# Performance work log

Measured on AMD Instinct MI355X. Metric: run time of the kernel, lower is better.

The kernel has to match this reference:

```python
import jax, jax.numpy as jnp
import numpy as np

DIM_OUT = 64


def setup_inputs() -> dict:
    key = jax.random.key(0)
    k1, k2, k3, k4 = jax.random.split(key, 4)
    B, N, D_in, D_out = 4, 4096, 512, DIM_OUT
    x = jax.random.normal(k1, (B, N, D_in), dtype=jnp.float32)
    s = 1.0 / np.sqrt(D_in)
    Wk = jax.random.normal(k2, (D_out, D_in), dtype=jnp.float32) * s
    Wq = jax.random.normal(k3, (D_out, D_in), dtype=jnp.float32) * s
    Wv = jax.random.normal(k4, (D_out, D_in), dtype=jnp.float32) * s
    return {"x": x, "Wk": Wk, "Wq": Wq, "Wv": Wv}


def reference(x, Wk, Wq, Wv):
    # x: [B, N, D_in]; W*: [D_out, D_in] (torch Linear, no bias -> x @ W.T)
    keys = jnp.einsum('bnd,od->bno', x, Wk)
    queries = jnp.einsum('bnd,od->bno', x, Wq)
    values = jnp.einsum('bnd,od->bno', x, Wv)
    d_out = Wk.shape[0]
    # causal attention scores: [B, N, N]
    scores = jnp.einsum('bio,bjo->bij', queries, keys) / jnp.sqrt(jnp.float32(d_out))
    N = x.shape[1]
    causal = jnp.tril(jnp.ones((N, N), dtype=bool))  # [N, N]
    scores = jnp.where(causal[None, :, :], scores, -jnp.inf)
    att = jax.nn.softmax(scores, axis=-1)
    return jnp.einsum('bjo,bij->bio', values, att)
```

## Files before the change

kernel.cpp:

```cpp
#include <hip/hip_runtime.h>
#include <hip/hip_bf16.h>
#include <math.h>

#define N_   4096
#define DIN  512
#define D_   64

typedef __attribute__((ext_vector_type(8))) short  bf16x8;
typedef __attribute__((ext_vector_type(4))) float  f32x4;

__device__ __forceinline__ unsigned short bf16rne(float x) {
    unsigned u = __float_as_uint(x);
    return (unsigned short)((u + 0x7FFFu + ((u >> 16) & 1u)) >> 16);
}
__device__ __forceinline__ unsigned cvt2(float a, float b) {
    __hip_bfloat162 h = __float22bfloat162_rn(make_float2(a, b));
    unsigned u; __builtin_memcpy(&u, &h, 4);
    return u;
}
__device__ __forceinline__ uint2 cvt4(float4 v) {
    return make_uint2(cvt2(v.x, v.y), cvt2(v.z, v.w));
}
__device__ __forceinline__ int swz(int row, int byte_in_row) {
    return (row * 128 + (byte_in_row ^ ((row & 7) << 4))) >> 1;
}

__device__ __forceinline__ int pb64(int qi) {
    const int k = qi >> 4;
    return qi + 16 * (k * (k - 1) / 2) + (qi & 15) * k;
}

#define PART64_F 4160

__global__ __launch_bounds__(512) void proj_kernel(
    const float* __restrict__ X, const float* __restrict__ Wk,
    const float* __restrict__ Wq, const float* __restrict__ Wv,
    unsigned short* __restrict__ Kb, unsigned short* __restrict__ Qb,
    unsigned short* __restrict__ Vt)
{
    __shared__ unsigned short Xs[2][64 * 64];
    __shared__ unsigned short Ws[2][192 * 64];

    const int tid  = threadIdx.x;
    const int lane = tid & 63;
    const int w    = tid >> 6;
    const int q15  = lane & 15;
    const int hi   = lane >> 4;
    const int rt   = w >> 1;
    const int oh   = w & 1;
    const int rbase = blockIdx.x * 64;

    float4 xr[2], wr[6];

    auto loadT = [&](int kc) {
        #pragma unroll
        for (int i = 0; i < 2; ++i) {
            const int idx = tid + i * 512;
            xr[i] = *(const float4*)(X + (size_t)(rbase + (idx >> 4)) * DIN + kc + (idx & 15) * 4);
        }
        #pragma unroll
        for (int i = 0; i < 6; ++i) {
            const int idx  = tid + i * 512;
            const int wrow = idx >> 4;
            const float* Wp = (wrow < 64)  ? Wk + (size_t)wrow * DIN
                            : (wrow < 128) ? Wq + (size_t)(wrow - 64) * DIN
                                           : Wv + (size_t)(wrow - 128) * DIN;
            wr[i] = *(const float4*)(Wp + kc + (idx & 15) * 4);
        }
    };
    auto storeT = [&](int p) {
        #pragma unroll
        for (int i = 0; i < 2; ++i) {
            const int idx = tid + i * 512;
            *(uint2*)&Xs[p][swz(idx >> 4, (idx & 15) * 8)] = cvt4(xr[i]);
        }
        #pragma unroll
        for (int i = 0; i < 6; ++i) {
            const int idx = tid + i * 512;
            *(uint2*)&Ws[p][swz(idx >> 4, (idx & 15) * 8)] = cvt4(wr[i]);
        }
    };

    f32x4 acc[6];
    #pragma unroll
    for (int i = 0; i < 6; ++i) acc[i] = (f32x4){0.f, 0.f, 0.f, 0.f};

    loadT(0);
    int p = 0;
    for (int it = 0; it < 8; ++it) {
        storeT(p);
        __syncthreads();
        if (it < 7) loadT((it + 1) * 64);
        #pragma unroll
        for (int ks = 0; ks < 2; ++ks) {
            bf16x8 af = *(const bf16x8*)&Xs[p][swz(rt * 16 + q15, ks * 64 + hi * 16)];
            #pragma unroll
            for (int j = 0; j < 6; ++j) {
                bf16x8 bfr = *(const bf16x8*)&Ws[p][swz((oh * 6 + j) * 16 + q15, ks * 64 + hi * 16)];
                acc[j] = __builtin_amdgcn_mfma_f32_16x16x32_bf16(af, bfr, acc[j], 0, 0, 0);
            }
        }
        p ^= 1;
    }

    unsigned short* Os = &Ws[0][0];
    #pragma unroll
    for (int j = 0; j < 6; ++j) {
        const int og = oh * 6 + j;
        #pragma unroll
        for (int r = 0; r < 4; ++r) {
            const int n = rt * 16 + hi * 4 + r;
            const int o = og * 16 + q15;
            unsigned short v = bf16rne(acc[j][r]);
            if (og < 4)      Kb[(size_t)(rbase + n) * D_ + o]        = v;
            else if (og < 8) Qb[(size_t)(rbase + n) * D_ + (o - 64)] = v;
            else             Os[n * 66 + (o - 128)]                  = v;
        }
    }
    __syncthreads();
    {
        const int o  = tid >> 3;
        const int ng = (tid & 7) * 8;
        unsigned short tmp[8];
        #pragma unroll
        for (int i = 0; i < 8; ++i) tmp[i] = Os[(ng + i) * 66 + o];
        const int b  = rbase >> 12;
        const int nb = rbase & (N_ - 1);
        *(uint4*)(Vt + ((size_t)b * D_ + o) * N_ + nb + ng) = *(uint4*)&tmp[0];
    }
}

__global__ __launch_bounds__(256, 3) void attn_part_kernel(
    const unsigned short* __restrict__ Qb, const unsigned short* __restrict__ Kb,
    const unsigned short* __restrict__ Vt, float* __restrict__ Pws)
{
    __shared__ unsigned short Ks[2][64 * 64];
    __shared__ unsigned short Vs[2][64 * 64];
    __shared__ unsigned short Pb[4][16 * 64];

    const int tid  = threadIdx.x;
    const int lane = tid & 63;
    const int w    = tid >> 6;
    const int q15  = lane & 15;
    const int hi   = lane >> 4;

    const int b = blockIdx.x & 3;
    const int u = blockIdx.x >> 2;
    int sl, qi;
    if      (u < 64)  { sl = 0; qi = 63 - u; }
    else if (u < 112) { sl = 1; qi = 63 - (u - 64); }
    else if (u < 144) { sl = 2; qi = 63 - (u - 112); }
    else              { sl = 3; qi = 63 - (u - 144); }
    const int nch  = qi + 1;
    const int cbeg = sl * 16;
    const int cend = min(nch, cbeg + 16);

    const unsigned short* Qp = Qb + (size_t)b * N_ * D_;
    const unsigned short* Kp = Kb + (size_t)b * N_ * D_;
    const unsigned short* Vp = Vt + (size_t)b * D_ * N_;

    const int qg = qi * 64 + w * 16 + q15;
    bf16x8 qf[2];
    #pragma unroll
    for (int ks = 0; ks < 2; ++ks)
        qf[ks] = *(const bf16x8*)(Qp + (size_t)qg * D_ + ks * 32 + hi * 8);

    f32x4 accO[4];
    #pragma unroll
    for (int dt = 0; dt < 4; ++dt) accO[dt] = (f32x4){0.f, 0.f, 0.f, 0.f};
    float lsum = 0.f;

    const int srow = tid >> 2;
    const int sb0  = (tid & 3) * 32;
    uint4 kr0, kr1, vr0, vr1;

    auto loadC = [&](int c) {
        const int kb2 = c * 64;
        const unsigned short* kp = Kp + (size_t)(kb2 + srow) * D_ + sb0 / 2;
        kr0 = *(const uint4*)kp;
        kr1 = *(const uint4*)(kp + 8);
        const unsigned short* vp = Vp + (size_t)srow * N_ + kb2 + sb0 / 2;
        vr0 = *(const uint4*)vp;
        vr1 = *(const uint4*)(vp + 8);
    };
    auto writeC = [&](int p) {
        *(uint4*)&Ks[p][swz(srow, sb0)]      = kr0;
        *(uint4*)&Ks[p][swz(srow, sb0 + 16)] = kr1;
        *(uint4*)&Vs[p][swz(srow, sb0)]      = vr0;
        *(uint4*)&Vs[p][swz(srow, sb0 + 16)] = vr1;
    };

    loadC(cbeg);
    writeC(0);
    __syncthreads();

    unsigned short* Pw = &Pb[w][0];
    const float SC = 0.125f * 1.44269504f;
    int p = 0;

    for (int c = cbeg; c < cend; ++c) {
        const int kbase = c * 64;
        if (c + 1 < cend) loadC(c + 1);

        f32x4 sv[4];
        #pragma unroll
        for (int kt = 0; kt < 4; ++kt) {
            bf16x8 k0 = *(const bf16x8*)&Ks[p][swz(kt * 16 + q15, hi * 16)];
            bf16x8 k1 = *(const bf16x8*)&Ks[p][swz(kt * 16 + q15, 64 + hi * 16)];
            sv[kt] = __builtin_amdgcn_mfma_f32_16x16x32_bf16(k0, qf[0], (f32x4){0.f,0.f,0.f,0.f}, 0, 0, 0);
            sv[kt] = __builtin_amdgcn_mfma_f32_16x16x32_bf16(k1, qf[1], sv[kt], 0, 0, 0);
        }

        #pragma unroll
        for (int kt = 0; kt < 4; ++kt) {
            float pv[4];
            #pragma unroll
            for (int r = 0; r < 4; ++r) {
                float v = sv[kt][r] * SC;
                const int kg = kbase + kt * 16 + hi * 4 + r;
                v = (kg <= qg) ? v : -INFINITY;
                pv[r] = __builtin_amdgcn_exp2f(v);
                lsum += pv[r];
            }
            *(uint2*)&Pw[swz(q15, kt * 32 + hi * 8)] =
                make_uint2(cvt2(pv[0], pv[1]), cvt2(pv[2], pv[3]));
        }

        #pragma unroll
        for (int ks2 = 0; ks2 < 2; ++ks2) {
            bf16x8 pf = *(const bf16x8*)&Pw[swz(q15, ks2 * 64 + hi * 16)];
            #pragma unroll
            for (int dt = 0; dt < 4; ++dt) {
                bf16x8 vf = *(const bf16x8*)&Vs[p][swz(dt * 16 + q15, ks2 * 64 + hi * 16)];
                accO[dt] = __builtin_amdgcn_mfma_f32_16x16x32_bf16(vf, pf, accO[dt], 0, 0, 0);
            }
        }

        __syncthreads();
        if (c + 1 < cend) writeC(p ^ 1);
        __syncthreads();
        p ^= 1;
    }

    lsum += __shfl_xor(lsum, 16);
    lsum += __shfl_xor(lsum, 32);

    float* partO = Pws + ((size_t)b * 160 + pb64(qi) + sl) * PART64_F;
    #pragma unroll
    for (int dt = 0; dt < 4; ++dt)
        #pragma unroll
        for (int r = 0; r < 4; ++r)
            partO[(dt * 16 + hi * 4 + r) * 64 + w * 16 + q15] = accO[dt][r];
    if (hi == 0) partO[4096 + w * 16 + q15] = lsum;
}

__global__ __launch_bounds__(256) void attn_merge_kernel(
    const float* __restrict__ Pws, float* __restrict__ O)
{
    __shared__ float Tr[64 * 68];
    __shared__ float Ls[64];

    const int tid = threadIdx.x;
    const int b   = blockIdx.x & 3;
    const int qi  = blockIdx.x >> 2;
    const int np  = (qi + 16) >> 4;
    const float* base = Pws + ((size_t)b * 160 + pb64(qi)) * PART64_F;

    {
        const int d  = tid >> 2;
        const int qg = (tid & 3) * 16;
        float s[16];
        #pragma unroll
        for (int i = 0; i < 16; ++i) s[i] = 0.f;
        for (int pp = 0; pp < np; ++pp) {
            const float* sp = base + (size_t)pp * PART64_F + d * 64 + qg;
            #pragma unroll
            for (int i = 0; i < 4; ++i) {
                float4 v = *(const float4*)(sp + i * 4);
                s[4*i]   += v.x; s[4*i+1] += v.y;
                s[4*i+2] += v.z; s[4*i+3] += v.w;
            }
        }
        #pragma unroll
        for (int i = 0; i < 16; ++i) Tr[d * 68 + qg + i] = s[i];
    }
    if (tid < 64) {
        float L = 0.f;
        for (int pp = 0; pp < np; ++pp) L += base[(size_t)pp * PART64_F + 4096 + tid];
        Ls[tid] = 1.0f / L;
    }
    __syncthreads();
    {
        const int q  = tid >> 2;
        const int dg = (tid & 3) * 16;
        const float rL = Ls[q];
        float ov[16];
        #pragma unroll
        for (int i = 0; i < 16; ++i) ov[i] = Tr[(dg + i) * 68 + q] * rL;
        float* dst = O + ((size_t)b * N_ + qi * 64 + q) * D_ + dg;
        #pragma unroll
        for (int i = 0; i < 4; ++i)
            *(float4*)(dst + i * 4) = make_float4(ov[4*i], ov[4*i+1], ov[4*i+2], ov[4*i+3]);
    }
}

extern "C" void kernel_launch(void* const* d_in, const int* in_sizes, int n_in,
                              void* d_out, int out_size, void* d_ws, size_t ws_size,
                              hipStream_t stream)
{
    const float* x  = (const float*)d_in[0];
    const float* Wk = (const float*)d_in[1];
    const float* Wq = (const float*)d_in[2];
    const float* Wv = (const float*)d_in[3];
    float* O = (float*)d_out;

    const size_t per = (size_t)4 * N_ * D_;
    unsigned short* Kb = (unsigned short*)d_ws;
    unsigned short* Qb = Kb + per;
    unsigned short* Vt = Qb + per;
    float* Pws = (float*)((char*)d_ws + 3 * per * sizeof(unsigned short));

    proj_kernel<<<dim3(4 * N_ / 64), 512, 0, stream>>>(x, Wk, Wq, Wv, Kb, Qb, Vt);
    attn_part_kernel<<<dim3(640), 256, 0, stream>>>(Qb, Kb, Vt, Pws);
    attn_merge_kernel<<<dim3(256), 256, 0, stream>>>(Pws, O);
}
```

Baseline: 51.56 us.

## Use 128-query attention tiles with direct global-to-LDS K/V loads

Each attention block now covers 128 query rows instead of 64, with each wave handling two 16-row query tiles. Every K/V chunk staged in shared memory therefore feeds twice as many MFMAs, halving K/V traffic per query. K/V chunks are loaded with global_load_lds straight into pre-swizzled LDS, replacing register staging and dropping one barrier per iteration. The causal mask is applied only on the diagonal chunks. The partial-sum layout and the merge kernel are reworked for 128-row tiles. The trade-off is half as many blocks (320 partial, 128 merge), which may leave CUs idle or unbalanced, plus higher register and LDS use per block.

```diff
diff --git a/kernel.cpp b/kernel.cpp
--- a/kernel.cpp
+++ b/kernel.cpp
@@ -8,6 +8,8 @@
 
 typedef __attribute__((ext_vector_type(8))) short  bf16x8;
 typedef __attribute__((ext_vector_type(4))) float  f32x4;
+
+#define ZERO4 ((f32x4){0.f, 0.f, 0.f, 0.f})
 
 __device__ __forceinline__ unsigned short bf16rne(float x) {
     unsigned u = __float_as_uint(x);
@@ -25,12 +27,16 @@
     return (row * 128 + (byte_in_row ^ ((row & 7) << 4))) >> 1;
 }
 
-__device__ __forceinline__ int pb64(int qi) {
-    const int k = qi >> 4;
-    return qi + 16 * (k * (k - 1) / 2) + (qi & 15) * k;
-}
-
-#define PART64_F 4160
+#define GLD16(gp, lp)                                                          \
+    __builtin_amdgcn_global_load_lds(                                          \
+        (const __attribute__((address_space(1))) unsigned int*)(gp),           \
+        (__attribute__((address_space(3))) unsigned int*)(lp), 16, 0, 0)
+
+__device__ __forceinline__ int pb128(int qi) {
+    const int g = qi >> 3, r = qi & 7;
+    return 4 * g * (g + 1) + r * (g + 1);
+}
+#define PART128_F 8320
 
 __global__ __launch_bounds__(512) void proj_kernel(
     const float* __restrict__ X, const float* __restrict__ Wk,
@@ -83,7 +89,7 @@
 
     f32x4 acc[6];
     #pragma unroll
-    for (int i = 0; i < 6; ++i) acc[i] = (f32x4){0.f, 0.f, 0.f, 0.f};
+    for (int i = 0; i < 6; ++i) acc[i] = ZERO4;
 
     loadT(0);
     int p = 0;
@@ -130,13 +136,13 @@
     }
 }
 
-__global__ __launch_bounds__(256, 3) void attn_part_kernel(
+__global__ __launch_bounds__(256) void attn_part_kernel(
     const unsigned short* __restrict__ Qb, const unsigned short* __restrict__ Kb,
     const unsigned short* __restrict__ Vt, float* __restrict__ Pws)
 {
     __shared__ unsigned short Ks[2][64 * 64];
     __shared__ unsigned short Vs[2][64 * 64];
-    __shared__ unsigned short Pb[4][16 * 64];
+    __shared__ unsigned short Pb[4][32 * 64];
 
     const int tid  = threadIdx.x;
     const int lane = tid & 63;
@@ -147,51 +153,47 @@
     const int b = blockIdx.x & 3;
     const int u = blockIdx.x >> 2;
     int sl, qi;
-    if      (u < 64)  { sl = 0; qi = 63 - u; }
-    else if (u < 112) { sl = 1; qi = 63 - (u - 64); }
-    else if (u < 144) { sl = 2; qi = 63 - (u - 112); }
-    else              { sl = 3; qi = 63 - (u - 144); }
-    const int nch  = qi + 1;
+    if      (u < 32) { sl = 0; qi = 31 - u; }
+    else if (u < 56) { sl = 1; qi = 31 - (u - 32); }
+    else if (u < 72) { sl = 2; qi = 31 - (u - 56); }
+    else             { sl = 3; qi = 31 - (u - 72); }
+    const int nch  = 2 * qi + 2;
     const int cbeg = sl * 16;
     const int cend = min(nch, cbeg + 16);
+    const int qb   = qi * 128;
 
     const unsigned short* Qp = Qb + (size_t)b * N_ * D_;
     const unsigned short* Kp = Kb + (size_t)b * N_ * D_;
     const unsigned short* Vp = Vt + (size_t)b * D_ * N_;
 
-    const int qg = qi * 64 + w * 16 + q15;
-    bf16x8 qf[2];
-    #pragma unroll
-    for (int ks = 0; ks < 2; ++ks)
-        qf[ks] = *(const bf16x8*)(Qp + (size_t)qg * D_ + ks * 32 + hi * 8);
-
-    f32x4 accO[4];
-    #pragma unroll
-    for (int dt = 0; dt < 4; ++dt) accO[dt] = (f32x4){0.f, 0.f, 0.f, 0.f};
-    float lsum = 0.f;
-
-    const int srow = tid >> 2;
-    const int sb0  = (tid & 3) * 32;
-    uint4 kr0, kr1, vr0, vr1;
-
-    auto loadC = [&](int c) {
+    bf16x8 qf[2][2];
+    #pragma unroll
+    for (int qq = 0; qq < 2; ++qq)
+        #pragma unroll
+        for (int ks = 0; ks < 2; ++ks)
+            qf[qq][ks] = *(const bf16x8*)(Qp + (size_t)(qb + w * 32 + qq * 16 + q15) * D_ + ks * 32 + hi * 8);
+
+    f32x4 accO[2][4];
+    #pragma unroll
+    for (int qq = 0; qq < 2; ++qq)
+        #pragma unroll
+        for (int dt = 0; dt < 4; ++dt) accO[qq][dt] = ZERO4;
+    float lsum[2] = {0.f, 0.f};
+
+    const int lsw = 8 * ((lane & 7) ^ (lane >> 3));
+
+    auto issueChunk = [&](int p, int c) {
         const int kb2 = c * 64;
-        const unsigned short* kp = Kp + (size_t)(kb2 + srow) * D_ + sb0 / 2;
-        kr0 = *(const uint4*)kp;
-        kr1 = *(const uint4*)(kp + 8);
-        const unsigned short* vp = Vp + (size_t)srow * N_ + kb2 + sb0 / 2;
-        vr0 = *(const uint4*)vp;
-        vr1 = *(const uint4*)(vp + 8);
+        #pragma unroll
+        for (int i = 0; i < 2; ++i) {
+            const int r8  = w * 2 + i;
+            const int row = r8 * 8 + (lane >> 3);
+            GLD16(Kp + (size_t)(kb2 + row) * D_ + lsw, &Ks[p][r8 * 512]);
+            GLD16(Vp + (size_t)row * N_ + kb2 + lsw,   &Vs[p][r8 * 512]);
+        }
     };
-    auto writeC = [&](int p) {
-        *(uint4*)&Ks[p][swz(srow, sb0)]      = kr0;
-        *(uint4*)&Ks[p][swz(srow, sb0 + 16)] = kr1;
-        *(uint4*)&Vs[p][swz(srow, sb0)]      = vr0;
-        *(uint4*)&Vs[p][swz(srow, sb0 + 16)] = vr1;
-    };
-
-    loadC(cbeg);
-    writeC(0);
+
+    issueChunk(0, cbeg);
     __syncthreads();
 
     unsigned short* Pw = &Pb[w][0];
@@ -199,108 +201,126 @@
     int p = 0;
 
     for (int c = cbeg; c < cend; ++c) {
+        if (c + 1 < cend) issueChunk(p ^ 1, c + 1);
         const int kbase = c * 64;
-        if (c + 1 < cend) loadC(c + 1);
-
-        f32x4 sv[4];
+        const bool edge = (c >= nch - 2);
+
+        f32x4 sv[2][4];
         #pragma unroll
         for (int kt = 0; kt < 4; ++kt) {
             bf16x8 k0 = *(const bf16x8*)&Ks[p][swz(kt * 16 + q15, hi * 16)];
             bf16x8 k1 = *(const bf16x8*)&Ks[p][swz(kt * 16 + q15, 64 + hi * 16)];
-            sv[kt] = __builtin_amdgcn_mfma_f32_16x16x32_bf16(k0, qf[0], (f32x4){0.f,0.f,0.f,0.f}, 0, 0, 0);
-            sv[kt] = __builtin_amdgcn_mfma_f32_16x16x32_bf16(k1, qf[1], sv[kt], 0, 0, 0);
-        }
-
-        #pragma unroll
-        for (int kt = 0; kt < 4; ++kt) {
-            float pv[4];
-            #pragma unroll
-            for (int r = 0; r < 4; ++r) {
-                float v = sv[kt][r] * SC;
-                const int kg = kbase + kt * 16 + hi * 4 + r;
-                v = (kg <= qg) ? v : -INFINITY;
-                pv[r] = __builtin_amdgcn_exp2f(v);
-                lsum += pv[r];
+            sv[0][kt] = __builtin_amdgcn_mfma_f32_16x16x32_bf16(k0, qf[0][0], ZERO4, 0, 0, 0);
+            sv[0][kt] = __builtin_amdgcn_mfma_f32_16x16x32_bf16(k1, qf[0][1], sv[0][kt], 0, 0, 0);
+            sv[1][kt] = __builtin_amdgcn_mfma_f32_16x16x32_bf16(k0, qf[1][0], ZERO4, 0, 0, 0);
+            sv[1][kt] = __builtin_amdgcn_mfma_f32_16x16x32_bf16(k1, qf[1][1], sv[1][kt], 0, 0, 0);
+        }
+
+        #pragma unroll
+        for (int qq = 0; qq < 2; ++qq) {
+            const int qg = qb + w * 32 + qq * 16 + q15;
+            #pragma unroll
+            for (int kt = 0; kt < 4; ++kt) {
+                float pv[4];
+                #pragma unroll
+                for (int r = 0; r < 4; ++r) {
+                    float v = sv[qq][kt][r] * SC;
+                    const int kg = kbase + kt * 16 + hi * 4 + r;
+                    if (edge) v = (kg <= qg) ? v : -INFINITY;
+                    pv[r] = __builtin_amdgcn_exp2f(v);
+                    lsum[qq] += pv[r];
+                }
+                *(uint2*)&Pw[swz(qq * 16 + q15, kt * 32 + hi * 8)] =
+                    make_uint2(cvt2(pv[0], pv[1]), cvt2(pv[2], pv[3]));
             }
-            *(uint2*)&Pw[swz(q15, kt * 32 + hi * 8)] =
-                make_uint2(cvt2(pv[0], pv[1]), cvt2(pv[2], pv[3]));
         }
 
         #pragma unroll
         for (int ks2 = 0; ks2 < 2; ++ks2) {
-            bf16x8 pf = *(const bf16x8*)&Pw[swz(q15, ks2 * 64 + hi * 16)];
-            #pragma unroll
-            for (int dt = 0; dt < 4; ++dt) {
-                bf16x8 vf = *(const bf16x8*)&Vs[p][swz(dt * 16 + q15, ks2 * 64 + hi * 16)];
-                accO[dt] = __builtin_amdgcn_mfma_f32_16x16x32_bf16(vf, pf, accO[dt], 0, 0, 0);
+            bf16x8 vf[4];
+            #pragma unroll
+            for (int dt = 0; dt < 4; ++dt)
+                vf[dt] = *(const bf16x8*)&Vs[p][swz(dt * 16 + q15, ks2 * 64 + hi * 16)];
+            #pragma unroll
+            for (int qq = 0; qq < 2; ++qq) {
+                bf16x8 pf = *(const bf16x8*)&Pw[swz(qq * 16 + q15, ks2 * 64 + hi * 16)];
+                #pragma unroll
+                for (int dt = 0; dt < 4; ++dt)
+                    accO[qq][dt] = __builtin_amdgcn_mfma_f32_16x16x32_bf16(vf[dt], pf, accO[qq][dt], 0, 0, 0);
             }
         }
 
-        __syncthreads();
-        if (c + 1 < cend) writeC(p ^ 1);
         __syncthreads();
         p ^= 1;
     }
 
-    lsum += __shfl_xor(lsum, 16);
-    lsum += __shfl_xor(lsum, 32);
-
-    float* partO = Pws + ((size_t)b * 160 + pb64(qi) + sl) * PART64_F;
-    #pragma unroll
-    for (int dt = 0; dt < 4; ++dt)
-        #pragma unroll
-        for (int r = 0; r < 4; ++r)
-            partO[(dt * 16 + hi * 4 + r) * 64 + w * 16 + q15] = accO[dt][r];
-    if (hi == 0) partO[4096 + w * 16 + q15] = lsum;
+    #pragma unroll
+    for (int qq = 0; qq < 2; ++qq) {
+        lsum[qq] += __shfl_xor(lsum[qq], 16);
+        lsum[qq] += __shfl_xor(lsum[qq], 32);
+    }
+
+    float* partO = Pws + ((size_t)b * 80 + pb128(qi) + sl) * PART128_F;
+    #pragma unroll
+    for (int qq = 0; qq < 2; ++qq) {
+        #pragma unroll
+        for (int dt = 0; dt < 4; ++dt)
+            #pragma unroll
+            for (int r = 0; r < 4; ++r)
+                partO[(dt * 16 + hi * 4 + r) * 128 + w * 32 + qq * 16 + q15] = accO[qq][dt][r];
+        if (hi == 0) partO[8192 + w * 32 + qq * 16 + q15] = lsum[qq];
+    }
 }
 
 __global__ __launch_bounds__(256) void attn_merge_kernel(
     const float* __restrict__ Pws, float* __restrict__ O)
 {
-    __shared__ float Tr[64 * 68];
-    __shared__ float Ls[64];
+    __shared__ float Tr[64 * 132];
+    __shared__ float Ls[128];
 
     const int tid = threadIdx.x;
     const int b   = blockIdx.x & 3;
     const int qi  = blockIdx.x >> 2;
-    const int np  = (qi + 16) >> 4;
-    const float* base = Pws + ((size_t)b * 160 + pb64(qi)) * PART64_F;
+    const int np  = (qi >> 3) + 1;
+    const float* base = Pws + ((size_t)b * 80 + pb128(qi)) * PART128_F;
 
     {
         const int d  = tid >> 2;
-        const int qg = (tid & 3) * 16;
-        float s[16];
-        #pragma unroll
-        for (int i = 0; i < 16; ++i) s[i] = 0.f;
+        const int qg = (tid & 3) * 32;
+        float s[32];
+        #pragma unroll
+        for (int i = 0; i < 32; ++i) s[i] = 0.f;
         for (int pp = 0; pp < np; ++pp) {
-            const float* sp = base + (size_t)pp * PART64_F + d * 64 + qg;
-            #pragma unroll
-            for (int i = 0; i < 4; ++i) {
+            const float* sp = base + (size_t)pp * PART128_F + d * 128 + qg;
+            #pragma unroll
+            for (int i = 0; i < 8; ++i) {
                 float4 v = *(const float4*)(sp + i * 4);
                 s[4*i]   += v.x; s[4*i+1] += v.y;
                 s[4*i+2] += v.z; s[4*i+3] += v.w;
             }
         }
         #pragma unroll
-        for (int i = 0; i < 16; ++i) Tr[d * 68 + qg + i] = s[i];
-    }
-    if (tid < 64) {
+        for (int i = 0; i < 32; ++i) Tr[d * 132 + qg + i] = s[i];
+    }
+    if (tid < 128) {
         float L = 0.f;
-        for (int pp = 0; pp < np; ++pp) L += base[(size_t)pp * PART64_F + 4096 + tid];
+        for (int pp = 0; pp < np; ++pp) L += base[(size_t)pp * PART128_F + 8192 + tid];
         Ls[tid] = 1.0f / L;
     }
     __syncthreads();
     {
-        const int q  = tid >> 2;
-        const int dg = (tid & 3) * 16;
+        const int q  = tid >> 1;
+        const int dg = (tid & 1) * 32;
         const float rL = Ls[q];
-        float ov[16];
-        #pragma unroll
-        for (int i = 0; i < 16; ++i) ov[i] = Tr[(dg + i) * 68 + q] * rL;
-        float* dst = O + ((size_t)b * N_ + qi * 64 + q) * D_ + dg;
-        #pragma unroll
-        for (int i = 0; i < 4; ++i)
-            *(float4*)(dst + i * 4) = make_float4(ov[4*i], ov[4*i+1], ov[4*i+2], ov[4*i+3]);
+        float* dst = O + ((size_t)b * N_ + qi * 128 + q) * D_ + dg;
+        #pragma unroll
+        for (int i = 0; i < 8; ++i) {
+            float4 v = make_float4(Tr[(dg + 4*i    ) * 132 + q] * rL,
+                                   Tr[(dg + 4*i + 1) * 132 + q] * rL,
+                                   Tr[(dg + 4*i + 2) * 132 + q] * rL,
+                                   Tr[(dg + 4*i + 3) * 132 + q] * rL);
+            *(float4*)(dst + i * 4) = v;
+        }
     }
 }
 
@@ -321,6 +341,6 @@
     float* Pws = (float*)((char*)d_ws + 3 * per * sizeof(unsigned short));
 
     proj_kernel<<<dim3(4 * N_ / 64), 512, 0, stream>>>(x, Wk, Wq, Wv, Kb, Qb, Vt);
-    attn_part_kernel<<<dim3(640), 256, 0, stream>>>(Qb, Kb, Vt, Pws);
-    attn_merge_kernel<<<dim3(256), 256, 0, stream>>>(Pws, O);
-}
+    attn_part_kernel<<<dim3(320), 256, 0, stream>>>(Qb, Kb, Vt, Pws);
+    attn_merge_kernel<<<dim3(128), 256, 0, stream>>>(Pws, O);
+}
```

After: 62.80 us. +21.8%, slower.

## Load K/V via direct global-to-LDS, keep P in registers with permlane swaps

Applied to the files above, without the earlier changes.

The attention kernel now streams K and V tiles with global_load_lds straight into shared memory, which removes the register staging and one barrier per chunk. The P tile stays in registers and is reshuffled with permlane swaps instead of going through an LDS buffer. The PV MFMA operand order is swapped so partial outputs are stored row-major, which lets the merge kernel drop its LDS transpose. Causal masking now runs only on the diagonal chunk. The swizzle for the direct loads and the lane permutation must match exactly, and dropping the occupancy hint may change register allocation.

```diff
diff --git a/kernel.cpp b/kernel.cpp
--- a/kernel.cpp
+++ b/kernel.cpp
@@ -8,6 +8,8 @@
 
 typedef __attribute__((ext_vector_type(8))) short  bf16x8;
 typedef __attribute__((ext_vector_type(4))) float  f32x4;
+
+#define ZERO4 ((f32x4){0.f, 0.f, 0.f, 0.f})
 
 __device__ __forceinline__ unsigned short bf16rne(float x) {
     unsigned u = __float_as_uint(x);
@@ -21,15 +23,25 @@
 __device__ __forceinline__ uint2 cvt4(float4 v) {
     return make_uint2(cvt2(v.x, v.y), cvt2(v.z, v.w));
 }
+__device__ __forceinline__ void pl32swap(unsigned &a, unsigned &b) {
+    asm volatile("v_permlane32_swap_b32 %0, %1" : "+v"(a), "+v"(b));
+}
+__device__ __forceinline__ void pl16swap(unsigned &a, unsigned &b) {
+    asm volatile("v_permlane16_swap_b32 %0, %1" : "+v"(a), "+v"(b));
+}
 __device__ __forceinline__ int swz(int row, int byte_in_row) {
     return (row * 128 + (byte_in_row ^ ((row & 7) << 4))) >> 1;
 }
+
+#define GLD16(gp, lp)                                                          \
+    __builtin_amdgcn_global_load_lds(                                          \
+        (const __attribute__((address_space(1))) unsigned int*)(gp),           \
+        (__attribute__((address_space(3))) unsigned int*)(lp), 16, 0, 0)
 
 __device__ __forceinline__ int pb64(int qi) {
     const int k = qi >> 4;
     return qi + 16 * (k * (k - 1) / 2) + (qi & 15) * k;
 }
-
 #define PART64_F 4160
 
 __global__ __launch_bounds__(512) void proj_kernel(
@@ -83,7 +95,7 @@
 
     f32x4 acc[6];
     #pragma unroll
-    for (int i = 0; i < 6; ++i) acc[i] = (f32x4){0.f, 0.f, 0.f, 0.f};
+    for (int i = 0; i < 6; ++i) acc[i] = ZERO4;
 
     loadT(0);
     int p = 0;
@@ -130,13 +142,12 @@
     }
 }
 
-__global__ __launch_bounds__(256, 3) void attn_part_kernel(
+__global__ __launch_bounds__(256) void attn_part_kernel(
     const unsigned short* __restrict__ Qb, const unsigned short* __restrict__ Kb,
     const unsigned short* __restrict__ Vt, float* __restrict__ Pws)
 {
     __shared__ unsigned short Ks[2][64 * 64];
     __shared__ unsigned short Vs[2][64 * 64];
-    __shared__ unsigned short Pb[4][16 * 64];
 
     const int tid  = threadIdx.x;
     const int lane = tid & 63;
@@ -154,12 +165,13 @@
     const int nch  = qi + 1;
     const int cbeg = sl * 16;
     const int cend = min(nch, cbeg + 16);
+    const int qb   = qi * 64;
 
     const unsigned short* Qp = Qb + (size_t)b * N_ * D_;
     const unsigned short* Kp = Kb + (size_t)b * N_ * D_;
     const unsigned short* Vp = Vt + (size_t)b * D_ * N_;
 
-    const int qg = qi * 64 + w * 16 + q15;
+    const int qg = qb + w * 16 + q15;
     bf16x8 qf[2];
     #pragma unroll
     for (int ks = 0; ks < 2; ++ks)
@@ -167,77 +179,76 @@
 
     f32x4 accO[4];
     #pragma unroll
-    for (int dt = 0; dt < 4; ++dt) accO[dt] = (f32x4){0.f, 0.f, 0.f, 0.f};
+    for (int dt = 0; dt < 4; ++dt) accO[dt] = ZERO4;
     float lsum = 0.f;
 
-    const int srow = tid >> 2;
-    const int sb0  = (tid & 3) * 32;
-    uint4 kr0, kr1, vr0, vr1;
-
-    auto loadC = [&](int c) {
+    const int lsw = 8 * ((lane & 7) ^ (lane >> 3));
+
+    auto issueChunk = [&](int p, int c) {
         const int kb2 = c * 64;
-        const unsigned short* kp = Kp + (size_t)(kb2 + srow) * D_ + sb0 / 2;
-        kr0 = *(const uint4*)kp;
-        kr1 = *(const uint4*)(kp + 8);
-        const unsigned short* vp = Vp + (size_t)srow * N_ + kb2 + sb0 / 2;
-        vr0 = *(const uint4*)vp;
-        vr1 = *(const uint4*)(vp + 8);
+        #pragma unroll
+        for (int i = 0; i < 2; ++i) {
+            const int r8  = w * 2 + i;
+            const int row = r8 * 8 + (lane >> 3);
+            GLD16(Kp + (size_t)(kb2 + row) * D_ + lsw, &Ks[p][r8 * 512]);
+            GLD16(Vp + (size_t)row * N_ + kb2 + lsw,   &Vs[p][r8 * 512]);
+        }
     };
-    auto writeC = [&](int p) {
-        *(uint4*)&Ks[p][swz(srow, sb0)]      = kr0;
-        *(uint4*)&Ks[p][swz(srow, sb0 + 16)] = kr1;
-        *(uint4*)&Vs[p][swz(srow, sb0)]      = vr0;
-        *(uint4*)&Vs[p][swz(srow, sb0 + 16)] = vr1;
-    };
-
-    loadC(cbeg);
-    writeC(0);
+
+    issueChunk(0, cbeg);
     __syncthreads();
 
-    unsigned short* Pw = &Pb[w][0];
     const float SC = 0.125f * 1.44269504f;
     int p = 0;
 
     for (int c = cbeg; c < cend; ++c) {
+        if (c + 1 < cend) issueChunk(p ^ 1, c + 1);
         const int kbase = c * 64;
-        if (c + 1 < cend) loadC(c + 1);
+        const bool edge = (c == nch - 1);
 
         f32x4 sv[4];
         #pragma unroll
         for (int kt = 0; kt < 4; ++kt) {
             bf16x8 k0 = *(const bf16x8*)&Ks[p][swz(kt * 16 + q15, hi * 16)];
             bf16x8 k1 = *(const bf16x8*)&Ks[p][swz(kt * 16 + q15, 64 + hi * 16)];
-            sv[kt] = __builtin_amdgcn_mfma_f32_16x16x32_bf16(k0, qf[0], (f32x4){0.f,0.f,0.f,0.f}, 0, 0, 0);
+            sv[kt] = __builtin_amdgcn_mfma_f32_16x16x32_bf16(k0, qf[0], ZERO4, 0, 0, 0);
             sv[kt] = __builtin_amdgcn_mfma_f32_16x16x32_bf16(k1, qf[1], sv[kt], 0, 0, 0);
         }
 
+        unsigned pk[4][2];
         #pragma unroll
         for (int kt = 0; kt < 4; ++kt) {
             float pv[4];
             #pragma unroll
             for (int r = 0; r < 4; ++r) {
-                float v = sv[kt][r] * SC;
+                float vv = sv[kt][r] * SC;
                 const int kg = kbase + kt * 16 + hi * 4 + r;
-                v = (kg <= qg) ? v : -INFINITY;
-                pv[r] = __builtin_amdgcn_exp2f(v);
+                if (edge) vv = (kg <= qg) ? vv : -INFINITY;
+                pv[r] = __builtin_amdgcn_exp2f(vv);
                 lsum += pv[r];
             }
-            *(uint2*)&Pw[swz(q15, kt * 32 + hi * 8)] =
-                make_uint2(cvt2(pv[0], pv[1]), cvt2(pv[2], pv[3]));
+            pk[kt][0] = cvt2(pv[0], pv[1]);
+            pk[kt][1] = cvt2(pv[2], pv[3]);
         }
 
         #pragma unroll
         for (int ks2 = 0; ks2 < 2; ++ks2) {
-            bf16x8 pf = *(const bf16x8*)&Pw[swz(q15, ks2 * 64 + hi * 16)];
+            unsigned a0 = pk[2 * ks2][0],     a1 = pk[2 * ks2][1];
+            unsigned b0 = pk[2 * ks2 + 1][0], b1 = pk[2 * ks2 + 1][1];
+            pl32swap(a0, b0);
+            pl32swap(a1, b1);
+            pl16swap(a0, b0);
+            pl16swap(a1, b1);
+            unsigned pw[4] = {a0, a1, b0, b1};
+            bf16x8 pa;
+            __builtin_memcpy(&pa, pw, 16);
             #pragma unroll
             for (int dt = 0; dt < 4; ++dt) {
                 bf16x8 vf = *(const bf16x8*)&Vs[p][swz(dt * 16 + q15, ks2 * 64 + hi * 16)];
-                accO[dt] = __builtin_amdgcn_mfma_f32_16x16x32_bf16(vf, pf, accO[dt], 0, 0, 0);
+                accO[dt] = __builtin_amdgcn_mfma_f32_16x16x32_bf16(pa, vf, accO[dt], 0, 0, 0);
             }
         }
 
-        __syncthreads();
-        if (c + 1 < cend) writeC(p ^ 1);
         __syncthreads();
         p ^= 1;
     }
@@ -250,58 +261,42 @@
     for (int dt = 0; dt < 4; ++dt)
         #pragma unroll
         for (int r = 0; r < 4; ++r)
-            partO[(dt * 16 + hi * 4 + r) * 64 + w * 16 + q15] = accO[dt][r];
+            partO[(w * 16 + hi * 4 + r) * 64 + dt * 16 + q15] = accO[dt][r];
     if (hi == 0) partO[4096 + w * 16 + q15] = lsum;
 }
 
 __global__ __launch_bounds__(256) void attn_merge_kernel(
     const float* __restrict__ Pws, float* __restrict__ O)
 {
-    __shared__ float Tr[64 * 68];
-    __shared__ float Ls[64];
-
     const int tid = threadIdx.x;
     const int b   = blockIdx.x & 3;
     const int qi  = blockIdx.x >> 2;
     const int np  = (qi + 16) >> 4;
     const float* base = Pws + ((size_t)b * 160 + pb64(qi)) * PART64_F;
 
-    {
-        const int d  = tid >> 2;
-        const int qg = (tid & 3) * 16;
-        float s[16];
-        #pragma unroll
-        for (int i = 0; i < 16; ++i) s[i] = 0.f;
-        for (int pp = 0; pp < np; ++pp) {
-            const float* sp = base + (size_t)pp * PART64_F + d * 64 + qg;
-            #pragma unroll
-            for (int i = 0; i < 4; ++i) {
-                float4 v = *(const float4*)(sp + i * 4);
-                s[4*i]   += v.x; s[4*i+1] += v.y;
-                s[4*i+2] += v.z; s[4*i+3] += v.w;
-            }
-        }
-        #pragma unroll
-        for (int i = 0; i < 16; ++i) Tr[d * 68 + qg + i] = s[i];
-    }
-    if (tid < 64) {
-        float L = 0.f;
-        for (int pp = 0; pp < np; ++pp) L += base[(size_t)pp * PART64_F + 4096 + tid];
-        Ls[tid] = 1.0f / L;
-    }
-    __syncthreads();
-    {
-        const int q  = tid >> 2;
-        const int dg = (tid & 3) * 16;
-        const float rL = Ls[q];
-        float ov[16];
-        #pragma unroll
-        for (int i = 0; i < 16; ++i) ov[i] = Tr[(dg + i) * 68 + q] * rL;
-        float* dst = O + ((size_t)b * N_ + qi * 64 + q) * D_ + dg;
-        #pragma unroll
-        for (int i = 0; i < 4; ++i)
-            *(float4*)(dst + i * 4) = make_float4(ov[4*i], ov[4*i+1], ov[4*i+2], ov[4*i+3]);
-    }
+    const int q  = tid >> 2;
+    const int dg = (tid & 3) * 16;
+
+    float s[16];
+    #pragma unroll
+    for (int i = 0; i < 16; ++i) s[i] = 0.f;
+    float L = 0.f;
+    for (int pp = 0; pp < np; ++pp) {
+        const float* sp = base + (size_t)pp * PART64_F + q * 64 + dg;
+        #pragma unroll
+        for (int i = 0; i < 4; ++i) {
+            float4 v = *(const float4*)(sp + i * 4);
+            s[4*i]   += v.x; s[4*i+1] += v.y;
+            s[4*i+2] += v.z; s[4*i+3] += v.w;
+        }
+        L += base[(size_t)pp * PART64_F + 4096 + q];
+    }
+    const float rL = 1.0f / L;
+    float* dst = O + ((size_t)b * N_ + qi * 64 + q) * D_ + dg;
+    #pragma unroll
+    for (int i = 0; i < 4; ++i)
+        *(float4*)(dst + i * 4) = make_float4(s[4*i] * rL, s[4*i+1] * rL,
+                                              s[4*i+2] * rL, s[4*i+3] * rL);
 }
 
 extern "C" void kernel_launch(void* const* d_in, const int* in_sizes, int n_in,
```

Result: faster. 50.49 us (-2.1%).
